# Performance work log

Measured on AMD Instinct MI355X. Metric: run time of the kernel, lower is better.

Reference implementation:

```python
import jax, jax.numpy as jnp
import numpy as np

N, K = 20000, 32
M = 100000
IN_F, DIM_W, ATT = 256, 64, 128


def setup_inputs() -> dict:
    key = jax.random.key(0)
    ks = jax.random.split(key, 9)
    ev = jax.random.normal(ks[0], (N, IN_F), dtype=jnp.float32)
    ej = jax.random.normal(ks[1], (M, IN_F), dtype=jnp.float32)
    ew = jax.random.normal(ks[2], (M, DIM_W), dtype=jnp.float32)
    v_j = jax.random.randint(ks[3], (N, K), 0, M + 1, dtype=jnp.int32)
    v_w = jax.random.randint(ks[4], (N, K), 0, M + 1, dtype=jnp.int32)
    # learned parameters (uninitialized Tensors in torch; use small randn)
    W_1 = jax.random.normal(ks[5], (IN_F + DIM_W, ATT), dtype=jnp.float32) * 0.05
    W_2 = jax.random.normal(ks[6], (IN_F, ATT), dtype=jnp.float32) * 0.05
    b = jax.random.normal(ks[7], (1, ATT), dtype=jnp.float32) * 0.05
    v = jax.random.normal(ks[8], (1, ATT), dtype=jnp.float32) * 0.05
    return {"ev": ev, "ej": ej, "ew": ew, "v_j": v_j, "v_w": v_w,
            "W_1": W_1, "W_2": W_2, "b": b, "v": v}


def reference(ev, ej, ew, v_j, v_w, W_1, W_2, b, v):
    # prepend zero padding row so index 0 acts as "no neighbor"
    ej_p = jnp.concatenate([jnp.zeros((1, ej.shape[1]), ej.dtype), ej], axis=0)   # [M+1, F]
    ew_p = jnp.concatenate([jnp.zeros((1, ew.shape[1]), ew.dtype), ew], axis=0)   # [M+1, Dw]
    eNj = ej_p[v_j]                                   # [N, K, F]
    eNw = ew_p[v_w]                                   # [N, K, Dw]
    k = v_j.shape[1]
    eNv = jnp.broadcast_to(ev[:, None, :], (ev.shape[0], k, ev.shape[1]))  # [N, K, F]
    eN_vw = jnp.concatenate([eNv, eNw], axis=-1)      # [N, K, F+Dw]
    av_j = (jnp.einsum('nkf,fa->nka', eN_vw, W_1)
            + jnp.einsum('nkf,fa->nka', eNj, W_2) + b)  # [N, K, A]
    x = jnp.einsum('nka,a->nk', jax.nn.relu(av_j), v[0])[..., None]  # [N, K, 1]
    a = jax.nn.softmax(x, axis=1)                     # softmax over neighbor dim
    eN = jnp.sum(a * eNj, axis=1)                     # [N, F]
    return eN
```

## Files before the change

kernel.cpp:

```cpp
#include <hip/hip_runtime.h>
#include <hip/hip_bf16.h>
#include <type_traits>

#define N_ROWS 20000
#define KNBR   32
#define M_ROWS 100000
#define INF    256
#define DIMW   64

#define GRID_J ((M_ROWS + 63) / 64)
#define GRID_V ((N_ROWS + 63) / 64)

typedef __attribute__((ext_vector_type(8))) short short8v;
typedef __attribute__((ext_vector_type(4))) float f32x4;
typedef __attribute__((ext_vector_type(2))) float f32x2;

__device__ __forceinline__ float bfu(unsigned short s) {
    return __uint_as_float((unsigned)s << 16);
}
__device__ __forceinline__ unsigned short f2b(float x) {
    union { __hip_bfloat16 h; unsigned short u; } cv;
    cv.h = __float2bfloat16(x);
    return cv.u;
}
__device__ __forceinline__ unsigned pk2(float a, float b) {
    return (unsigned)f2b(a) | ((unsigned)f2b(b) << 16);
}

__global__ void prep_wt(const float* __restrict__ W2, const float* __restrict__ W1w,
                        const float* __restrict__ W1v,
                        unsigned short* __restrict__ WtJ, unsigned short* __restrict__ WtW,
                        unsigned short* __restrict__ WtV,
                        unsigned short* __restrict__ tabJ, unsigned short* __restrict__ tabW)
{
    int idx = blockIdx.x * 256 + threadIdx.x;
    if (idx < 128 * 256) {
        int c = idx >> 8, k = idx & 255;
        WtJ[idx] = f2b(W2[k * 128 + c]);
    } else if (idx < 128 * 256 + 128 * 64) {
        int i2 = idx - 128 * 256;
        int c = i2 >> 6, k = i2 & 63;
        WtW[i2] = f2b(W1w[k * 128 + c]);
    } else if (idx < 2 * 128 * 256 + 128 * 64) {
        int i3 = idx - (128 * 256 + 128 * 64);
        int c = i3 >> 8, k = i3 & 255;
        WtV[i3] = f2b(W1v[k * 128 + c]);
    }
    if (idx < 128) { tabJ[idx] = 0; tabW[idx] = 0; }
}

template <int F, bool WRITE_AH, bool BIAS>
__device__ __forceinline__ void gemm_body(
    const float* __restrict__ A, const unsigned short* __restrict__ Wt,
    unsigned short* __restrict__ outB, unsigned short* __restrict__ Ah,
    const float* __restrict__ bias, int R, int rowOffset, int m0,
    unsigned short* __restrict__ As,
    unsigned short* __restrict__ Ws,
    unsigned short* __restrict__ Tile)
{
    const int t   = threadIdx.x;
    const int wid = t >> 6;
    const int l   = t & 63;
    const int l15 = l & 15;
    const int l4  = l >> 4;
    const int wr  = wid >> 1;
    const int wc  = wid & 1;

    f32x4 acc[2][4];
    #pragma unroll
    for (int rg = 0; rg < 2; rg++)
        #pragma unroll
        for (int ct = 0; ct < 4; ct++) acc[rg][ct] = (f32x4){0.f, 0.f, 0.f, 0.f};

    const int ar  = t >> 2;
    const int ac  = (t & 3) * 16;
    const int wrS = t >> 1;
    const int wcS = (t & 1) * 32;

    for (int k0 = 0; k0 < F; k0 += 64) {
        {
            int r = m0 + ar;
            unsigned pk[8];
            if (r < R) {
                const float* ap = A + (size_t)r * F + k0 + ac;
                #pragma unroll
                for (int q = 0; q < 4; q++) {
                    f32x4 f = *(const f32x4*)(ap + q * 4);
                    pk[q * 2 + 0] = pk2(f.x, f.y);
                    pk[q * 2 + 1] = pk2(f.z, f.w);
                }
                if (WRITE_AH) {
                    uint4 lo = {pk[0], pk[1], pk[2], pk[3]};
                    uint4 hi = {pk[4], pk[5], pk[6], pk[7]};
                    *(uint4*)(Ah + (size_t)r * F + k0 + ac)     = lo;
                    *(uint4*)(Ah + (size_t)r * F + k0 + ac + 8) = hi;
                }
            } else {
                #pragma unroll
                for (int q = 0; q < 8; q++) pk[q] = 0u;
            }
            int base = ar * 128 + ac * 2;
            int swz  = (ar & 7) << 4;
            uint4 lo = {pk[0], pk[1], pk[2], pk[3]};
            uint4 hi = {pk[4], pk[5], pk[6], pk[7]};
            *(uint4*)((char*)As + ((base)      ^ swz)) = lo;
            *(uint4*)((char*)As + ((base + 16) ^ swz)) = hi;
        }
        {
            const unsigned short* wp = Wt + (size_t)wrS * F + k0 + wcS;
            int base = wrS * 128 + wcS * 2;
            int swz  = (wrS & 7) << 4;
            #pragma unroll
            for (int q = 0; q < 4; q++) {
                uint4 wv = *(const uint4*)(wp + q * 8);
                *(uint4*)((char*)Ws + ((base + q * 16) ^ swz)) = wv;
            }
        }
        __syncthreads();

        short8v afrag[2][2];
        #pragma unroll
        for (int rg = 0; rg < 2; rg++) {
            int arow = wr * 32 + rg * 16 + l15;
            int aswz = (arow & 7) << 4;
            #pragma unroll
            for (int ks = 0; ks < 2; ks++) {
                int boff = arow * 128 + (ks * 32 + l4 * 8) * 2;
                afrag[rg][ks] = *(const short8v*)((const char*)As + (boff ^ aswz));
            }
        }
        #pragma unroll
        for (int ct = 0; ct < 4; ct++) {
            int bcol = wc * 64 + ct * 16 + l15;
            int bswz = (bcol & 7) << 4;
            #pragma unroll
            for (int ks = 0; ks < 2; ks++) {
                int boff = bcol * 128 + (ks * 32 + l4 * 8) * 2;
                short8v bfrag = *(const short8v*)((const char*)Ws + (boff ^ bswz));
                #pragma unroll
                for (int rg = 0; rg < 2; rg++)
                    acc[rg][ct] = __builtin_amdgcn_mfma_f32_16x16x32_bf16(afrag[rg][ks], bfrag, acc[rg][ct], 0, 0, 0);
            }
        }
        __syncthreads();
    }

    #pragma unroll
    for (int rg = 0; rg < 2; rg++)
        #pragma unroll
        for (int ct = 0; ct < 4; ct++) {
            int col = wc * 64 + ct * 16 + l15;
            float bb = BIAS ? bias[col] : 0.f;
            #pragma unroll
            for (int i = 0; i < 4; i++)
                Tile[(wr * 32 + rg * 16 + l4 * 4 + i) * 136 + col] = f2b(acc[rg][ct][i] + bb);
        }
    __syncthreads();
    {
        int row = t >> 2, part = t & 3;
        int gr = m0 + row;
        if (gr < R) {
            unsigned short* op = outB + (size_t)(gr + rowOffset) * 128 + part * 32;
            const unsigned short* tp = Tile + row * 136 + part * 32;
            #pragma unroll
            for (int q = 0; q < 4; q++)
                *(uint4*)(op + q * 8) = *(const uint4*)(tp + q * 8);
        }
    }
    __syncthreads();
}

__global__ __launch_bounds__(256) void tables_fused(
    const float* __restrict__ ej, const float* __restrict__ ew,
    const float* __restrict__ ev,
    const unsigned short* __restrict__ WtJ, const unsigned short* __restrict__ WtW,
    const unsigned short* __restrict__ WtV,
    unsigned short* __restrict__ tabJ, unsigned short* __restrict__ tabW,
    unsigned short* __restrict__ evW1, unsigned short* __restrict__ ejh,
    const float* __restrict__ bias)
{
    __shared__ __align__(16) unsigned short As[64 * 64];
    __shared__ __align__(16) unsigned short Ws[128 * 64];
    __shared__ __align__(16) unsigned short Tile[64 * 136];

    const int bid = blockIdx.x;
    if (bid < GRID_J) {
        const int m0 = bid * 64;
        gemm_body<INF,  true,  false>(ej, WtJ, tabJ, ejh,     nullptr, M_ROWS, 1, m0, As, Ws, Tile);
        gemm_body<DIMW, false, false>(ew, WtW, tabW, nullptr, nullptr, M_ROWS, 1, m0, As, Ws, Tile);
    } else {
        const int m0 = (bid - GRID_J) * 64;
        gemm_body<INF,  false, true >(ev, WtV, evW1, nullptr, bias,    N_ROWS, 0, m0, As, Ws, Tile);
    }
}

__global__ __launch_bounds__(256) void score_out(
    const unsigned short* __restrict__ tabJ, const unsigned short* __restrict__ tabW,
    const unsigned short* __restrict__ evW1, const unsigned short* __restrict__ ejh,
    const int* __restrict__ vj, const int* __restrict__ vw,
    const float* __restrict__ vvec, float* __restrict__ out)
{
    const int n = blockIdx.x;
    const int t = threadIdx.x;

    __shared__ float  s_ev[128];
    __shared__ float  s_v[128];
    __shared__ int    s_j[32];
    __shared__ int    s_w[32];
    __shared__ float  s_a[32];
    __shared__ float2 s_red[2][128];

    if (t < 128) {
        s_ev[t] = bfu(evW1[(size_t)n * 128 + t]);
        s_v[t]  = vvec[t];
    } else if (t < 160) {
        int k = t - 128;
        s_j[k] = vj[n * KNBR + k];
        s_w[k] = vw[n * KNBR + k];
    }
    __syncthreads();

    const int k  = t >> 3;
    const int cg = t & 7;
    const int j  = s_j[k];
    const int w  = s_w[k];

    float x = 0.f;
    {
        const uint4* tj4 = (const uint4*)(tabJ + (size_t)j * 128 + cg * 16);
        const uint4* tw4 = (const uint4*)(tabW + (size_t)w * 128 + cg * 16);
        uint4 ja0 = tj4[0], ja1 = tj4[1];
        uint4 wa0 = tw4[0], wa1 = tw4[1];
        unsigned jw[8] = {ja0.x, ja0.y, ja0.z, ja0.w, ja1.x, ja1.y, ja1.z, ja1.w};
        unsigned ww[8] = {wa0.x, wa0.y, wa0.z, wa0.w, wa1.x, wa1.y, wa1.z, wa1.w};
        #pragma unroll
        for (int p = 0; p < 8; p++) {
            int c0 = cg * 16 + p * 2;
            float av0 = s_ev[c0]     + bfu((unsigned short)(jw[p] & 0xffff))
                                     + bfu((unsigned short)(ww[p] & 0xffff));
            float av1 = s_ev[c0 + 1] + bfu((unsigned short)(jw[p] >> 16))
                                     + bfu((unsigned short)(ww[p] >> 16));
            x = fmaf(fmaxf(av0, 0.f), s_v[c0], x);
            x = fmaf(fmaxf(av1, 0.f), s_v[c0 + 1], x);
        }
    }
    x += __shfl_xor(x, 1);
    x += __shfl_xor(x, 2);
    x += __shfl_xor(x, 4);
    if (cg == 0) s_a[k] = x;
    __syncthreads();

    if (t < 32) {
        float xi = s_a[t];
        float mx = xi;
        #pragma unroll
        for (int m = 16; m >= 1; m >>= 1) mx = fmaxf(mx, __shfl_xor(mx, m));
        float e = __expf(xi - mx);
        float s = e;
        #pragma unroll
        for (int m = 16; m >= 1; m >>= 1) s += __shfl_xor(s, m);
        s_a[t] = e / s;
    }
    __syncthreads();

    const int p = t & 127;
    const int h = t >> 7;
    unsigned uu[16];
    float    aa[16];
    #pragma unroll
    for (int kk = 0; kk < 16; kk++) {
        int k2 = h * 16 + kk;
        int j2 = s_j[k2];
        aa[kk] = s_a[k2];
        uu[kk] = j2 ? *(const unsigned*)(ejh + (size_t)(j2 - 1) * 256 + p * 2) : 0u;
    }
    float2 accv = {0.f, 0.f};
    #pragma unroll
    for (int kk = 0; kk < 16; kk++) {
        accv.x = fmaf(aa[kk], bfu((unsigned short)(uu[kk] & 0xffff)), accv.x);
        accv.y = fmaf(aa[kk], bfu((unsigned short)(uu[kk] >> 16)),    accv.y);
    }
    s_red[h][p] = accv;
    __syncthreads();
    if (t < 128) {
        float2 a0 = s_red[0][t], a1 = s_red[1][t];
        f32x2 r = {a0.x + a1.x, a0.y + a1.y};
        __builtin_nontemporal_store(r, (f32x2*)(out + (size_t)n * 256 + t * 2));
    }
}

extern "C" void kernel_launch(void* const* d_in, const int* in_sizes, int n_in,
                              void* d_out, int out_size, void* d_ws, size_t ws_size,
                              hipStream_t stream)
{
    const float* ev = (const float*)d_in[0];
    const float* ej = (const float*)d_in[1];
    const float* ew = (const float*)d_in[2];
    const int*   vj = (const int*)d_in[3];
    const int*   vw = (const int*)d_in[4];
    const float* W1 = (const float*)d_in[5];
    const float* W2 = (const float*)d_in[6];
    const float* b  = (const float*)d_in[7];
    const float* v  = (const float*)d_in[8];
    float* out = (float*)d_out;

    const float* W1v = W1;
    const float* W1w = W1 + 256 * 128;

    unsigned short* tabJ = (unsigned short*)d_ws;
    unsigned short* tabW = tabJ + (size_t)(M_ROWS + 1) * 128;
    unsigned short* ejh  = tabW + (size_t)(M_ROWS + 1) * 128;
    unsigned short* evW1 = ejh  + (size_t)M_ROWS * 256;
    unsigned short* WtJ  = evW1 + (size_t)N_ROWS * 128;
    unsigned short* WtW  = WtJ  + 128 * 256;
    unsigned short* WtV  = WtW  + 128 * 64;

    prep_wt<<<288, 256, 0, stream>>>(W2, W1w, W1v, WtJ, WtW, WtV, tabJ, tabW);
    tables_fused<<<GRID_J + GRID_V, 256, 0, stream>>>(ej, ew, ev, WtJ, WtW, WtV,
                                                      tabJ, tabW, evW1, ejh, b);
    score_out<<<N_ROWS, 256, 0, stream>>>(tabJ, tabW, evW1, ejh, vj, vw, v, out);
}
```

Measured before the change: 148.2 us.

## Process one row per wavefront in score kernel, removing LDS and barriers

The score/output kernel now assigns one 64-lane wavefront per output row, four rows per block, instead of one 256-thread block per row. Neighbour indices are exchanged with shuffles rather than shared memory, softmax runs entirely within the wave, and the weighted gather is done by each lane for 4 output columns across all 32 neighbours, so all __syncthreads and LDS staging go away. The v vector is pre-packed to bf16 in the prep kernel and read as vectors. In exchange each lane does more serial work (32 sequential gathers), which lowers memory-level parallelism per row, and v is now rounded to bf16.

```diff
diff --git a/kernel.cpp b/kernel.cpp
--- a/kernel.cpp
+++ b/kernel.cpp
@@ -14,6 +14,7 @@
 typedef __attribute__((ext_vector_type(8))) short short8v;
 typedef __attribute__((ext_vector_type(4))) float f32x4;
 typedef __attribute__((ext_vector_type(2))) float f32x2;
+typedef __attribute__((ext_vector_type(2))) unsigned u32x2;
 
 __device__ __forceinline__ float bfu(unsigned short s) {
     return __uint_as_float((unsigned)s << 16);
@@ -28,9 +29,9 @@
 }
 
 __global__ void prep_wt(const float* __restrict__ W2, const float* __restrict__ W1w,
-                        const float* __restrict__ W1v,
+                        const float* __restrict__ W1v, const float* __restrict__ v,
                         unsigned short* __restrict__ WtJ, unsigned short* __restrict__ WtW,
-                        unsigned short* __restrict__ WtV,
+                        unsigned short* __restrict__ WtV, unsigned* __restrict__ vh,
                         unsigned short* __restrict__ tabJ, unsigned short* __restrict__ tabW)
 {
     int idx = blockIdx.x * 256 + threadIdx.x;
@@ -47,6 +48,7 @@
         WtV[i3] = f2b(W1v[k * 128 + c]);
     }
     if (idx < 128) { tabJ[idx] = 0; tabW[idx] = 0; }
+    if (idx < 64)  { vh[idx] = pk2(v[2 * idx], v[2 * idx + 1]); }
 }
 
 template <int F, bool WRITE_AH, bool BIAS>
@@ -198,95 +200,72 @@
     const unsigned short* __restrict__ tabJ, const unsigned short* __restrict__ tabW,
     const unsigned short* __restrict__ evW1, const unsigned short* __restrict__ ejh,
     const int* __restrict__ vj, const int* __restrict__ vw,
-    const float* __restrict__ vvec, float* __restrict__ out)
-{
-    const int n = blockIdx.x;
-    const int t = threadIdx.x;
-
-    __shared__ float  s_ev[128];
-    __shared__ float  s_v[128];
-    __shared__ int    s_j[32];
-    __shared__ int    s_w[32];
-    __shared__ float  s_a[32];
-    __shared__ float2 s_red[2][128];
-
-    if (t < 128) {
-        s_ev[t] = bfu(evW1[(size_t)n * 128 + t]);
-        s_v[t]  = vvec[t];
-    } else if (t < 160) {
-        int k = t - 128;
-        s_j[k] = vj[n * KNBR + k];
-        s_w[k] = vw[n * KNBR + k];
-    }
-    __syncthreads();
-
-    const int k  = t >> 3;
-    const int cg = t & 7;
-    const int j  = s_j[k];
-    const int w  = s_w[k];
+    const unsigned* __restrict__ vh, float* __restrict__ out)
+{
+    const int wave = threadIdx.x >> 6;
+    const int l    = threadIdx.x & 63;
+    const int n    = blockIdx.x * 4 + wave;
+
+    int jv = 0, wv = 0;
+    if (l < 32) jv = vj[n * KNBR + l];
+    else        wv = vw[n * KNBR + (l - 32)];
+
+    const int k = l >> 1;
+    const int h = l & 1;
+    const int jk = __shfl(jv, k);
+    const int wk = __shfl(wv, 32 + k);
+
+    const uint4* tj4 = (const uint4*)(tabJ + (size_t)jk * 128 + h * 64);
+    const uint4* tw4 = (const uint4*)(tabW + (size_t)wk * 128 + h * 64);
+    const uint4* ev4 = (const uint4*)(evW1 + (size_t)n * 128 + h * 64);
+    const uint4* vv4 = (const uint4*)(vh + h * 32);
 
     float x = 0.f;
-    {
-        const uint4* tj4 = (const uint4*)(tabJ + (size_t)j * 128 + cg * 16);
-        const uint4* tw4 = (const uint4*)(tabW + (size_t)w * 128 + cg * 16);
-        uint4 ja0 = tj4[0], ja1 = tj4[1];
-        uint4 wa0 = tw4[0], wa1 = tw4[1];
-        unsigned jw[8] = {ja0.x, ja0.y, ja0.z, ja0.w, ja1.x, ja1.y, ja1.z, ja1.w};
-        unsigned ww[8] = {wa0.x, wa0.y, wa0.z, wa0.w, wa1.x, wa1.y, wa1.z, wa1.w};
-        #pragma unroll
-        for (int p = 0; p < 8; p++) {
-            int c0 = cg * 16 + p * 2;
-            float av0 = s_ev[c0]     + bfu((unsigned short)(jw[p] & 0xffff))
-                                     + bfu((unsigned short)(ww[p] & 0xffff));
-            float av1 = s_ev[c0 + 1] + bfu((unsigned short)(jw[p] >> 16))
-                                     + bfu((unsigned short)(ww[p] >> 16));
-            x = fmaf(fmaxf(av0, 0.f), s_v[c0], x);
-            x = fmaf(fmaxf(av1, 0.f), s_v[c0 + 1], x);
+    #pragma unroll
+    for (int q = 0; q < 8; q++) {
+        uint4 J = tj4[q], W = tw4[q], E = ev4[q], V = vv4[q];
+        unsigned ja[4] = {J.x, J.y, J.z, J.w};
+        unsigned wa[4] = {W.x, W.y, W.z, W.w};
+        unsigned ea[4] = {E.x, E.y, E.z, E.w};
+        unsigned va[4] = {V.x, V.y, V.z, V.w};
+        #pragma unroll
+        for (int p = 0; p < 4; p++) {
+            float av0 = bfu((unsigned short)(ea[p] & 0xffff))
+                      + bfu((unsigned short)(ja[p] & 0xffff))
+                      + bfu((unsigned short)(wa[p] & 0xffff));
+            float av1 = bfu((unsigned short)(ea[p] >> 16))
+                      + bfu((unsigned short)(ja[p] >> 16))
+                      + bfu((unsigned short)(wa[p] >> 16));
+            x = fmaf(fmaxf(av0, 0.f), bfu((unsigned short)(va[p] & 0xffff)), x);
+            x = fmaf(fmaxf(av1, 0.f), bfu((unsigned short)(va[p] >> 16)),    x);
         }
     }
     x += __shfl_xor(x, 1);
-    x += __shfl_xor(x, 2);
-    x += __shfl_xor(x, 4);
-    if (cg == 0) s_a[k] = x;
-    __syncthreads();
-
-    if (t < 32) {
-        float xi = s_a[t];
-        float mx = xi;
-        #pragma unroll
-        for (int m = 16; m >= 1; m >>= 1) mx = fmaxf(mx, __shfl_xor(mx, m));
-        float e = __expf(xi - mx);
-        float s = e;
-        #pragma unroll
-        for (int m = 16; m >= 1; m >>= 1) s += __shfl_xor(s, m);
-        s_a[t] = e / s;
-    }
-    __syncthreads();
-
-    const int p = t & 127;
-    const int h = t >> 7;
-    unsigned uu[16];
-    float    aa[16];
-    #pragma unroll
-    for (int kk = 0; kk < 16; kk++) {
-        int k2 = h * 16 + kk;
-        int j2 = s_j[k2];
-        aa[kk] = s_a[k2];
-        uu[kk] = j2 ? *(const unsigned*)(ejh + (size_t)(j2 - 1) * 256 + p * 2) : 0u;
-    }
-    float2 accv = {0.f, 0.f};
-    #pragma unroll
-    for (int kk = 0; kk < 16; kk++) {
-        accv.x = fmaf(aa[kk], bfu((unsigned short)(uu[kk] & 0xffff)), accv.x);
-        accv.y = fmaf(aa[kk], bfu((unsigned short)(uu[kk] >> 16)),    accv.y);
-    }
-    s_red[h][p] = accv;
-    __syncthreads();
-    if (t < 128) {
-        float2 a0 = s_red[0][t], a1 = s_red[1][t];
-        f32x2 r = {a0.x + a1.x, a0.y + a1.y};
-        __builtin_nontemporal_store(r, (f32x2*)(out + (size_t)n * 256 + t * 2));
-    }
+
+    float mx = x;
+    #pragma unroll
+    for (int m = 2; m <= 32; m <<= 1) mx = fmaxf(mx, __shfl_xor(mx, m));
+    float e = __expf(x - mx);
+    float s = e;
+    #pragma unroll
+    for (int m = 2; m <= 32; m <<= 1) s += __shfl_xor(s, m);
+    const float a = e / s;
+
+    float a0 = 0.f, a1 = 0.f, a2 = 0.f, a3 = 0.f;
+    #pragma unroll
+    for (int k2 = 0; k2 < KNBR; k2++) {
+        int   j2 = __shfl(jv, k2);
+        float ak = __shfl(a, k2 * 2);
+        int   jm = (j2 > 0) ? (j2 - 1) : 0;
+        float m2 = (j2 > 0) ? ak : 0.f;
+        u32x2 u  = *(const u32x2*)(ejh + (size_t)jm * 256 + l * 4);
+        a0 = fmaf(m2, bfu((unsigned short)(u.x & 0xffff)), a0);
+        a1 = fmaf(m2, bfu((unsigned short)(u.x >> 16)),    a1);
+        a2 = fmaf(m2, bfu((unsigned short)(u.y & 0xffff)), a2);
+        a3 = fmaf(m2, bfu((unsigned short)(u.y >> 16)),    a3);
+    }
+    f32x4 r = {a0, a1, a2, a3};
+    __builtin_nontemporal_store(r, (f32x4*)(out + (size_t)n * 256 + l * 4));
 }
 
 extern "C" void kernel_launch(void* const* d_in, const int* in_sizes, int n_in,
@@ -314,9 +293,10 @@
     unsigned short* WtJ  = evW1 + (size_t)N_ROWS * 128;
     unsigned short* WtW  = WtJ  + 128 * 256;
     unsigned short* WtV  = WtW  + 128 * 64;
-
-    prep_wt<<<288, 256, 0, stream>>>(W2, W1w, W1v, WtJ, WtW, WtV, tabJ, tabW);
+    unsigned*       vh   = (unsigned*)(WtV + 128 * 256);
+
+    prep_wt<<<288, 256, 0, stream>>>(W2, W1w, W1v, v, WtJ, WtW, WtV, vh, tabJ, tabW);
     tables_fused<<<GRID_J + GRID_V, 256, 0, stream>>>(ej, ew, ev, WtJ, WtW, WtV,
                                                       tabJ, tabW, evW1, ejh, b);
-    score_out<<<N_ROWS, 256, 0, stream>>>(tabJ, tabW, evW1, ejh, vj, vw, v, out);
-}
+    score_out<<<(N_ROWS + 3) / 4, 256, 0, stream>>>(tabJ, tabW, evW1, ejh, vj, vw, vh, out);
+}
```

New measurement: 207.1 us. 39.7% more time.
